# Kernel tuning notes

Hardware: AMD Instinct MI355X
Metric: run time of the kernel (lower is better)

## Reference

```python
import jax, jax.numpy as jnp
import numpy as np

DIM = 2048
HEADS = 16
HEAD_DIM = DIM // HEADS  # 128
FF = 8192
MAX_SEQ = 4096
B, S, PREV = 2, 2048, 1024
EPS = 1e-6
ROTARY_BASE = 10000.0


def setup_inputs() -> dict:
    key = jax.random.key(0)
    ks = jax.random.split(key, 16)
    n = lambda k, shape: jax.random.normal(k, shape, jnp.float32) * 0.02
    inp = {
        "x": jax.random.normal(ks[0], (B, S, DIM), jnp.float32),
        "k_cache": jax.random.normal(ks[1], (B, HEADS, PREV, HEAD_DIM), jnp.float32),
        "v_cache": jax.random.normal(ks[2], (B, HEADS, PREV, HEAD_DIM), jnp.float32),
        "attn_norm_w": jnp.ones((DIM,), jnp.float32),
        "ffn_norm_w": jnp.ones((DIM,), jnp.float32),
        "wq": n(ks[3], (DIM, DIM)), "bq": jnp.zeros((DIM,), jnp.float32),
        "wk": n(ks[4], (DIM, DIM)), "bk": jnp.zeros((DIM,), jnp.float32),
        "wv": n(ks[5], (DIM, DIM)), "bv": jnp.zeros((DIM,), jnp.float32),
        "wo": n(ks[6], (DIM, DIM)), "bo": jnp.zeros((DIM,), jnp.float32),
        "w_gate": n(ks[7], (DIM, FF)), "b_gate": jnp.zeros((FF,), jnp.float32),
        "w_val": n(ks[8], (DIM, FF)), "b_val": jnp.zeros((FF,), jnp.float32),
        "w_proj": n(ks[9], (FF, DIM)), "b_proj": jnp.zeros((DIM,), jnp.float32),
    }
    # precompute_freqs_cis as (cos, sin) pair: [MAX_SEQ, HEAD_DIM//2]
    freqs = 1.0 / (ROTARY_BASE ** (np.arange(0, HEAD_DIM, 2)[: HEAD_DIM // 2].astype(np.float32) / HEAD_DIM))
    ang = np.outer(np.arange(MAX_SEQ), freqs).astype(np.float32)
    inp["freqs_cos"] = jnp.asarray(np.cos(ang))
    inp["freqs_sin"] = jnp.asarray(np.sin(ang))
    inp["start_pos"] = PREV
    inp["cache_limit"] = 4096
    return inp


def rmsnorm(x, w):
    return x * jax.lax.rsqrt(jnp.mean(x * x, axis=-1, keepdims=True) + EPS) * w


def rope(x, cos, sin):
    # x: [B, H, S, D]; cos/sin: [1, 1, S, D/2] (complex multiply on even/odd pairs)
    xp = x.reshape(*x.shape[:-1], HEAD_DIM // 2, 2)
    x0, x1 = xp[..., 0], xp[..., 1]
    return jnp.stack([x0 * cos - x1 * sin, x0 * sin + x1 * cos], axis=-1).reshape(x.shape)


def reference(x, k_cache, v_cache, attn_norm_w, ffn_norm_w, wq, bq, wk, bk, wv, bv,
              wo, bo, w_gate, b_gate, w_val, b_val, w_proj, b_proj,
              freqs_cos, freqs_sin, start_pos, cache_limit):
    b, s, d = x.shape
    # --- attention block ---
    h = rmsnorm(x, attn_norm_w)
    split = lambda t: t.reshape(b, s, HEADS, HEAD_DIM).transpose(0, 2, 1, 3)
    q = split(h @ wq + bq)
    k = split(h @ wk + bk)
    v = split(h @ wv + bv)
    pos = (jnp.arange(s) + start_pos) % freqs_cos.shape[0]
    cos = freqs_cos[pos][None, None]  # [1,1,S,D/2]
    sin = freqs_sin[pos][None, None]
    q = rope(q, cos, sin)
    k = rope(k, cos, sin)
    # merge with KV cache (static python slicing for cache_limit)
    k_attn = jnp.concatenate([k_cache, k], axis=2)
    v_attn = jnp.concatenate([v_cache, v], axis=2)
    if cache_limit > 0:
        k_attn = k_attn[:, :, -cache_limit:, :]
        v_attn = v_attn[:, :, -cache_limit:, :]
    t_len = k_attn.shape[2]
    prev = t_len - s
    scores = jnp.einsum('bhsd,bhtd->bhst', q, k_attn) / np.float32(np.sqrt(HEAD_DIM))
    # causal mask: cache fully visible, current block lower-triangular
    allowed = jnp.arange(t_len)[None, :] <= (prev + jnp.arange(s))[:, None]
    scores = jnp.where(allowed, scores, jnp.finfo(scores.dtype).min)
    attn = jax.nn.softmax(scores, axis=-1)
    o = jnp.einsum('bhst,bhtd->bhsd', attn, v_attn).transpose(0, 2, 1, 3).reshape(b, s, d)
    x = x + (o @ wo + bo)
    # --- SwiGLU FFN block ---
    h = rmsnorm(x, ffn_norm_w)
    ff = (jax.nn.silu(h @ w_gate + b_gate) * (h @ w_val + b_val)) @ w_proj + b_proj
    x = x + ff
    return (x, k_attn, v_attn)
```

## Files before the change

### kernel.cpp

```cpp
#include <hip/hip_runtime.h>
#include <stdint.h>

typedef __bf16 bf16x8 __attribute__((ext_vector_type(8)));
typedef float  f32x4  __attribute__((ext_vector_type(4)));

__device__ __forceinline__ uint16_t f2b(float f) {
  uint32_t u = __float_as_uint(f);
  u += 0x7fffu + ((u >> 16) & 1u);
  return (uint16_t)(u >> 16);
}
__device__ __forceinline__ float b2f(uint16_t h) {
  return __uint_as_float(((uint32_t)h) << 16);
}

__device__ __forceinline__ void gl_lds16(const uint16_t* g, uint16_t* l) {
  __builtin_amdgcn_global_load_lds(
      (const __attribute__((address_space(1))) uint32_t*)g,
      (__attribute__((address_space(3))) uint32_t*)l, 16, 0, 0);
}

#define MFMA16(a,b,c) __builtin_amdgcn_mfma_f32_16x16x32_bf16((a),(b),(c),0,0,0)


__global__ __launch_bounds__(256)
void rmsnorm_k(const float* __restrict__ x, const float* __restrict__ w,
               uint16_t* __restrict__ out) {
  __shared__ float red[4];
  const int row = blockIdx.x, tid = threadIdx.x;
  const float* xr = x + (size_t)row * 2048;
  const int c = tid * 8;
  float4 a = *(const float4*)&xr[c];
  float4 b = *(const float4*)&xr[c + 4];
  float ss = a.x*a.x + a.y*a.y + a.z*a.z + a.w*a.w
           + b.x*b.x + b.y*b.y + b.z*b.z + b.w*b.w;
  ss += __shfl_xor(ss, 1);  ss += __shfl_xor(ss, 2);  ss += __shfl_xor(ss, 4);
  ss += __shfl_xor(ss, 8);  ss += __shfl_xor(ss, 16); ss += __shfl_xor(ss, 32);
  if ((tid & 63) == 0) red[tid >> 6] = ss;
  __syncthreads();
  const float tot = red[0] + red[1] + red[2] + red[3];
  const float rms = rsqrtf(tot * (1.0f / 2048.0f) + 1e-6f);
  float4 w0 = *(const float4*)&w[c];
  float4 w1 = *(const float4*)&w[c + 4];
  uint16_t* orow = out + (size_t)row * 2048;
  orow[c+0] = f2b(a.x * rms * w0.x); orow[c+1] = f2b(a.y * rms * w0.y);
  orow[c+2] = f2b(a.z * rms * w0.z); orow[c+3] = f2b(a.w * rms * w0.w);
  orow[c+4] = f2b(b.x * rms * w1.x); orow[c+5] = f2b(b.y * rms * w1.y);
  orow[c+6] = f2b(b.z * rms * w1.z); orow[c+7] = f2b(b.w * rms * w1.w);
}

__global__ void biascat_k(const float* __restrict__ bq, const float* __restrict__ bk,
                          const float* __restrict__ bv, float* __restrict__ out) {
  int i = blockIdx.x * 256 + threadIdx.x;
  if (i < 6144)
    out[i] = (i < 2048) ? bq[i] : ((i < 4096) ? bk[i - 2048] : bv[i - 4096]);
}

__global__ __launch_bounds__(256)
void transpose_k(const float* __restrict__ src, uint16_t* __restrict__ dst,
                 int K, int N) {
  __shared__ float tile[32][33];
  const int tx = threadIdx.x & 31, ty = threadIdx.x >> 5;
  const int n0 = blockIdx.x * 32, k0 = blockIdx.y * 32;
  #pragma unroll
  for (int i = 0; i < 4; ++i)
    tile[ty + i*8][tx] = src[(size_t)(k0 + ty + i*8) * N + n0 + tx];
  __syncthreads();
  #pragma unroll
  for (int i = 0; i < 4; ++i)
    dst[(size_t)(n0 + ty + i*8) * K + k0 + tx] = f2b(tile[tx][ty + i*8]);
}

__global__ __launch_bounds__(256)
void transpose_v_k(const float* __restrict__ src, uint16_t* __restrict__ dst) {
  __shared__ float tile[32][33];
  const int tx = threadIdx.x & 31, ty = threadIdx.x >> 5;
  const int t0 = blockIdx.x * 32, d0 = blockIdx.y * 32, bh = blockIdx.z;
  const float* s = src + (size_t)bh * 393216;
  uint16_t*   d = dst + (size_t)bh * 393216;
  #pragma unroll
  for (int i = 0; i < 4; ++i)
    tile[ty + i*8][tx] = s[(size_t)(t0 + ty + i*8) * 128 + d0 + tx];
  __syncthreads();
  #pragma unroll
  for (int i = 0; i < 4; ++i)
    d[(size_t)(d0 + ty + i*8) * 3072 + t0 + tx] = f2b(tile[tx][ty + i*8]);
}

__global__ __launch_bounds__(256)
void cvt_bf16_k(const float* __restrict__ src, uint16_t* __restrict__ dst) {
  const int i = blockIdx.x * 256 + threadIdx.x;
  float4 a = ((const float4*)src)[2*i];
  float4 b = ((const float4*)src)[2*i + 1];
  ushort4 lo, hi;
  lo.x = f2b(a.x); lo.y = f2b(a.y); lo.z = f2b(a.z); lo.w = f2b(a.w);
  hi.x = f2b(b.x); hi.y = f2b(b.y); hi.z = f2b(b.z); hi.w = f2b(b.w);
  ((ushort4*)dst)[2*i] = lo;
  ((ushort4*)dst)[2*i + 1] = hi;
}

__global__ __launch_bounds__(256)
void copy_cache_k(const float4* __restrict__ src, float4* __restrict__ dst) {
  const int idx = blockIdx.x * 256 + threadIdx.x;
  const int c4 = idx & 31, t = (idx >> 5) & 1023, bh = idx >> 15;
  dst[((size_t)bh * 3072 + t) * 32 + c4] = src[idx];
}

__global__ __launch_bounds__(256)
void rope_k(const uint16_t* __restrict__ qkv, const float* __restrict__ fc,
            const float* __restrict__ fs, uint16_t* __restrict__ qb,
            float* __restrict__ kat, float* __restrict__ vat) {
  const int bi = blockIdx.x;
  const int bs = bi >> 2;
  const int h  = ((bi & 3) << 2) + (threadIdx.x >> 6);
  const int d  = threadIdx.x & 63;
  const int b  = bs >> 11, s = bs & 2047;
  const int pos = s + 1024;
  const float c  = fc[pos * 64 + d];
  const float sn = fs[pos * 64 + d];
  const uint16_t* row = qkv + (size_t)bs * 6144 + h * 128;
  const float q0 = b2f(row[2*d]),        q1 = b2f(row[2*d + 1]);
  const float k0 = b2f(row[2048 + 2*d]), k1 = b2f(row[2048 + 2*d + 1]);
  const float v0 = b2f(row[4096 + 2*d]), v1 = b2f(row[4096 + 2*d + 1]);
  const size_t qo = (((size_t)b*16 + h) * 2048 + s) * 128 + 2*d;
  qb[qo]     = f2b(q0 * c - q1 * sn);
  qb[qo + 1] = f2b(q0 * sn + q1 * c);
  const size_t ko = (((size_t)b*16 + h) * 3072 + 1024 + s) * 128 + 2*d;
  kat[ko]     = k0 * c - k1 * sn;
  kat[ko + 1] = k0 * sn + k1 * c;
  vat[ko]     = v0;
  vat[ko + 1] = v1;
}

__global__ __launch_bounds__(256)
void attn_k(const uint16_t* __restrict__ qb, const uint16_t* __restrict__ kb,
            const uint16_t* __restrict__ vt, uint16_t* __restrict__ ob) {
  __shared__ __align__(16) uint16_t lsK[32 * 128];
  __shared__ __align__(16) uint16_t lsV[128 * 32];
  __shared__ __align__(16) uint16_t lsP[4][16 * 40];
  const int tid = threadIdx.x;
  const int lane = tid & 63, w = tid >> 6;
  const int l15 = lane & 15, q4 = lane >> 4;
  const int bh = blockIdx.x & 31;
  const int qi = 31 - (blockIdx.x >> 5);
  const int q0 = qi * 64;
  const int s_w = q0 + w * 16;

  int koff[2], voff[2];
  #pragma unroll
  for (int p = 0; p < 2; ++p) {
    const int idk = p * 256 + tid;
    const int krow = idk >> 4, kchp = idk & 15;
    koff[p] = krow * 128 + ((kchp ^ (krow & 15)) << 3);
    const int dd = idk >> 2, vch = idk & 3;
    voff[p] = dd * 3072 + (vch << 3);
  }
  const uint16_t* kbh = kb + (size_t)bh * 3072 * 128;
  const uint16_t* vbh = vt + (size_t)bh * 128 * 3072;

  bf16x8 qf[4];
  const uint16_t* qrow = qb + ((size_t)bh * 2048 + s_w + l15) * 128;
  #pragma unroll
  for (int kc = 0; kc < 4; ++kc)
    qf[kc] = *(const bf16x8*)&qrow[kc * 32 + q4 * 8];

  f32x4 o[8];
  #pragma unroll
  for (int nt = 0; nt < 8; ++nt) o[nt] = (f32x4){0.f, 0.f, 0.f, 0.f};
  float mrow[4], lrow[4];
  #pragma unroll
  for (int r = 0; r < 4; ++r) { mrow[r] = -1e38f; lrow[r] = 0.f; }

  const float SC = 0.08838834764831845f * 1.4426950408889634f;
  const int ntiles = (q0 + 1088) >> 5;
  const int limw = 1024 + s_w + 15;

  for (int tt = 0; tt < ntiles; ++tt) {
    const int t0 = tt << 5;
    __syncthreads();
    #pragma unroll
    for (int p = 0; p < 2; ++p) {
      gl_lds16(kbh + (size_t)t0 * 128 + koff[p], &lsK[(p * 256 + w * 64) * 8]);
      gl_lds16(vbh + t0 + voff[p],               &lsV[(p * 256 + w * 64) * 8]);
    }
    __syncthreads();
    if (t0 > limw) continue;

    f32x4 s0 = (f32x4){0.f,0.f,0.f,0.f}, s1 = (f32x4){0.f,0.f,0.f,0.f};
    #pragma unroll
    for (int kc = 0; kc < 4; ++kc) {
      const int chp = ((kc * 4 + q4) ^ l15) << 3;
      bf16x8 kf0 = *(const bf16x8*)&lsK[l15 * 128 + chp];
      bf16x8 kf1 = *(const bf16x8*)&lsK[(16 + l15) * 128 + chp];
      s0 = MFMA16(qf[kc], kf0, s0);
      s1 = MFMA16(qf[kc], kf1, s1);
    }
    if (t0 + 31 > 1024 + s_w) {
      #pragma unroll
      for (int r = 0; r < 4; ++r) {
        const int lim = 1024 + s_w + q4 * 4 + r;
        if (t0 + l15      > lim) s0[r] = -1e38f;
        if (t0 + 16 + l15 > lim) s1[r] = -1e38f;
      }
    }
    float alpha[4];
    #pragma unroll
    for (int r = 0; r < 4; ++r) {
      float v = fmaxf(s0[r], s1[r]);
      v = fmaxf(v, __shfl_xor(v, 1)); v = fmaxf(v, __shfl_xor(v, 2));
      v = fmaxf(v, __shfl_xor(v, 4)); v = fmaxf(v, __shfl_xor(v, 8));
      const float mn = fmaxf(mrow[r], v);
      alpha[r] = exp2f((mrow[r] - mn) * SC);
      mrow[r] = mn;
    }
    #pragma unroll
    for (int r = 0; r < 4; ++r) {
      const float nm = -mrow[r] * SC;
      const float p0 = exp2f(fmaf(s0[r], SC, nm));
      const float p1 = exp2f(fmaf(s1[r], SC, nm));
      float ps = p0 + p1;
      ps += __shfl_xor(ps, 1); ps += __shfl_xor(ps, 2);
      ps += __shfl_xor(ps, 4); ps += __shfl_xor(ps, 8);
      lrow[r] = fmaf(lrow[r], alpha[r], ps);
      lsP[w][(q4 * 4 + r) * 40 + l15]      = f2b(p0);
      lsP[w][(q4 * 4 + r) * 40 + 16 + l15] = f2b(p1);
    }
    #pragma unroll
    for (int nt = 0; nt < 8; ++nt)
      #pragma unroll
      for (int r = 0; r < 4; ++r) o[nt][r] *= alpha[r];
    bf16x8 pf = *(const bf16x8*)&lsP[w][l15 * 40 + q4 * 8];
    #pragma unroll
    for (int nt = 0; nt < 8; ++nt) {
      bf16x8 vf = *(const bf16x8*)&lsV[(nt * 16 + l15) * 32 + q4 * 8];
      o[nt] = MFMA16(pf, vf, o[nt]);
    }
  }
  const int b = bh >> 4, h = bh & 15;
  #pragma unroll
  for (int r = 0; r < 4; ++r) {
    const float inv = 1.0f / lrow[r];
    const int s = s_w + q4 * 4 + r;
    uint16_t* orow = ob + ((size_t)b * 2048 + s) * 2048 + h * 128;
    #pragma unroll
    for (int nt = 0; nt < 8; ++nt)
      orow[nt * 16 + l15] = f2b(o[nt][r] * inv);
  }
}

template <int EPI>
__global__ __launch_bounds__(256)
void gemm_k(const uint16_t* __restrict__ A, const uint16_t* __restrict__ Bt,
            const float* __restrict__ bias, const float* __restrict__ resid,
            const uint16_t* __restrict__ gbuf, void* __restrict__ outp,
            int M, int N, int K) {
  __shared__ __align__(16) uint16_t lsA[128 * 32];
  __shared__ __align__(16) uint16_t lsB[128 * 32];
  const int tid = threadIdx.x;
  const int lane = tid & 63, wvi = tid >> 6;
  const int l15 = lane & 15, q4 = lane >> 4;
  const int wm = wvi & 1, wn = wvi >> 1;
  const int m0 = blockIdx.y * 128, n0 = blockIdx.x * 128;
  const int lr = lane >> 2, lc = (lane & 3) << 3;

  f32x4 acc[4][4];
  #pragma unroll
  for (int i = 0; i < 4; ++i)
    #pragma unroll
    for (int j = 0; j < 4; ++j) acc[i][j] = (f32x4){0.f, 0.f, 0.f, 0.f};

  const uint16_t* Ab = A + (size_t)m0 * K;
  const uint16_t* Bb = Bt + (size_t)n0 * K;
  for (int k0 = 0; k0 < K; k0 += 32) {
    __syncthreads();
    #pragma unroll
    for (int p = 0; p < 2; ++p) {
      const int row = p * 64 + wvi * 16 + lr;
      gl_lds16(Ab + (size_t)row * K + k0 + lc, &lsA[(p * 256 + wvi * 64) * 8]);
      gl_lds16(Bb + (size_t)row * K + k0 + lc, &lsB[(p * 256 + wvi * 64) * 8]);
    }
    __syncthreads();
    bf16x8 af[4], bfr[4];
    #pragma unroll
    for (int i = 0; i < 4; ++i)
      af[i] = *(const bf16x8*)&lsA[(wm * 64 + i * 16 + l15) * 32 + q4 * 8];
    #pragma unroll
    for (int j = 0; j < 4; ++j)
      bfr[j] = *(const bf16x8*)&lsB[(wn * 64 + j * 16 + l15) * 32 + q4 * 8];
    #pragma unroll
    for (int i = 0; i < 4; ++i)
      #pragma unroll
      for (int j = 0; j < 4; ++j)
        acc[i][j] = MFMA16(af[i], bfr[j], acc[i][j]);
  }
  #pragma unroll
  for (int i = 0; i < 4; ++i) {
    #pragma unroll
    for (int j = 0; j < 4; ++j) {
      const int n = n0 + wn * 64 + j * 16 + l15;
      const float bn = bias[n];
      #pragma unroll
      for (int r = 0; r < 4; ++r) {
        const int m = m0 + wm * 64 + i * 16 + q4 * 4 + r;
        const size_t off = (size_t)m * N + n;
        const float v = acc[i][j][r] + bn;
        if (EPI == 0) {
          ((uint16_t*)outp)[off] = f2b(v);
        } else if (EPI == 1) {
          ((float*)outp)[off] = v + resid[off];
        } else {
          const float g = b2f(gbuf[off]);
          const float sg = g / (1.0f + __expf(-g));
          ((uint16_t*)outp)[off] = f2b(sg * v);
        }
      }
    }
  }
}

extern "C" void kernel_launch(void* const* d_in, const int* in_sizes, int n_in,
                              void* d_out, int out_size, void* d_ws, size_t ws_size,
                              hipStream_t stream) {
  const float* x   = (const float*)d_in[0];
  const float* kc  = (const float*)d_in[1];
  const float* vc  = (const float*)d_in[2];
  const float* anw = (const float*)d_in[3];
  const float* fnw = (const float*)d_in[4];
  const float* wq  = (const float*)d_in[5];
  const float* bq  = (const float*)d_in[6];
  const float* wk  = (const float*)d_in[7];
  const float* bk  = (const float*)d_in[8];
  const float* wv_ = (const float*)d_in[9];
  const float* bv  = (const float*)d_in[10];
  const float* wo  = (const float*)d_in[11];
  const float* bo  = (const float*)d_in[12];
  const float* wg  = (const float*)d_in[13];
  const float* bg  = (const float*)d_in[14];
  const float* wva = (const float*)d_in[15];
  const float* bva = (const float*)d_in[16];
  const float* wp  = (const float*)d_in[17];
  const float* bp  = (const float*)d_in[18];
  const float* fc  = (const float*)d_in[19];
  const float* fs  = (const float*)d_in[20];

  float* out_x = (float*)d_out;
  float* kat = out_x + 8388608;
  float* vat = kat + 12582912;

  char* ws = (char*)d_ws;
  uint16_t* h_b   = (uint16_t*)(ws);
  uint16_t* wbuf  = (uint16_t*)(ws + 16777216);
  uint16_t* qkv_b = (uint16_t*)(ws + 50331648);
  uint16_t* k_b   = (uint16_t*)(ws + 50331648);
  uint16_t* v_t   = (uint16_t*)(ws + 75497472);
  uint16_t* q_b   = (uint16_t*)(ws + 100663296);
  uint16_t* o_b   = (uint16_t*)(ws + 117440512);
  float*    x1    = (float*)   (ws + 134217728);
  float*    bcat  = (float*)   (ws + 167772160);
  uint16_t* g_b   = qkv_b;

  rmsnorm_k<<<4096, 256, 0, stream>>>(x, anw, h_b);
  biascat_k<<<24, 256, 0, stream>>>(bq, bk, bv, bcat);
  transpose_k<<<dim3(64, 64), 256, 0, stream>>>(wq,  wbuf,               2048, 2048);
  transpose_k<<<dim3(64, 64), 256, 0, stream>>>(wk,  wbuf + 1*2048*2048, 2048, 2048);
  transpose_k<<<dim3(64, 64), 256, 0, stream>>>(wv_, wbuf + 2*2048*2048, 2048, 2048);
  gemm_k<0><<<dim3(48, 32), 256, 0, stream>>>(h_b, wbuf, bcat, nullptr, nullptr,
                                              (void*)qkv_b, 4096, 6144, 2048);
  copy_cache_k<<<4096, 256, 0, stream>>>((const float4*)kc, (float4*)kat);
  copy_cache_k<<<4096, 256, 0, stream>>>((const float4*)vc, (float4*)vat);
  rope_k<<<16384, 256, 0, stream>>>(qkv_b, fc, fs, q_b, kat, vat);
  cvt_bf16_k<<<6144, 256, 0, stream>>>(kat, k_b);
  transpose_v_k<<<dim3(96, 4, 32), 256, 0, stream>>>(vat, v_t);
  attn_k<<<1024, 256, 0, stream>>>(q_b, k_b, v_t, o_b);
  transpose_k<<<dim3(64, 64), 256, 0, stream>>>(wo, wbuf, 2048, 2048);
  gemm_k<1><<<dim3(16, 32), 256, 0, stream>>>(o_b, wbuf, bo, x, nullptr,
                                              (void*)x1, 4096, 2048, 2048);
  rmsnorm_k<<<4096, 256, 0, stream>>>(x1, fnw, h_b);
  transpose_k<<<dim3(256, 64), 256, 0, stream>>>(wg, wbuf, 2048, 8192);
  gemm_k<0><<<dim3(64, 32), 256, 0, stream>>>(h_b, wbuf, bg, nullptr, nullptr,
                                              (void*)g_b, 4096, 8192, 2048);
  transpose_k<<<dim3(256, 64), 256, 0, stream>>>(wva, wbuf, 2048, 8192);
  gemm_k<2><<<dim3(64, 32), 256, 0, stream>>>(h_b, wbuf, bva, nullptr, g_b,
                                              (void*)g_b, 4096, 8192, 2048);
  transpose_k<<<dim3(64, 256), 256, 0, stream>>>(wp, wbuf, 8192, 2048);
  gemm_k<1><<<dim3(16, 32), 256, 0, stream>>>(g_b, wbuf, bp, x1, nullptr,
                                              (void*)out_x, 4096, 2048, 8192);
}
```

Measured before the change: 1.471 ms.

## Widen attention KV tile to 64, fuse K bf16 conversion into copy and rope

The attention kernel now processes 64 keys per tile instead of 32. It uses four score MFMAs and two PV MFMAs per d-tile, XOR-swizzles the V layout in LDS, defers the row-sum reduction to the end, and skips the output rescale when no lane's max changed. The separate fp32-to-bf16 pass over the whole K cache is removed: the bf16 K copy is now written directly by the cache-copy kernel and by rope_k, and the workspace buffers are relocated to fit. This cuts one full read and write of K and halves the number of attention barriers, at the cost of more LDS, more registers and more masked work on the diagonal tile.

```diff
diff --git a/kernel.cpp b/kernel.cpp
--- a/kernel.cpp
+++ b/kernel.cpp
@@ -87,18 +87,6 @@
 }
 
 __global__ __launch_bounds__(256)
-void cvt_bf16_k(const float* __restrict__ src, uint16_t* __restrict__ dst) {
-  const int i = blockIdx.x * 256 + threadIdx.x;
-  float4 a = ((const float4*)src)[2*i];
-  float4 b = ((const float4*)src)[2*i + 1];
-  ushort4 lo, hi;
-  lo.x = f2b(a.x); lo.y = f2b(a.y); lo.z = f2b(a.z); lo.w = f2b(a.w);
-  hi.x = f2b(b.x); hi.y = f2b(b.y); hi.z = f2b(b.z); hi.w = f2b(b.w);
-  ((ushort4*)dst)[2*i] = lo;
-  ((ushort4*)dst)[2*i + 1] = hi;
-}
-
-__global__ __launch_bounds__(256)
 void copy_cache_k(const float4* __restrict__ src, float4* __restrict__ dst) {
   const int idx = blockIdx.x * 256 + threadIdx.x;
   const int c4 = idx & 31, t = (idx >> 5) & 1023, bh = idx >> 15;
@@ -106,9 +94,23 @@
 }
 
 __global__ __launch_bounds__(256)
+void copy_cache_kb_k(const float4* __restrict__ src, float4* __restrict__ dst,
+                     uint16_t* __restrict__ dstb) {
+  const int idx = blockIdx.x * 256 + threadIdx.x;
+  const int c4 = idx & 31, t = (idx >> 5) & 1023, bh = idx >> 15;
+  float4 v = src[idx];
+  const size_t o = ((size_t)bh * 3072 + t) * 32 + c4;
+  dst[o] = v;
+  ushort4 b;
+  b.x = f2b(v.x); b.y = f2b(v.y); b.z = f2b(v.z); b.w = f2b(v.w);
+  ((ushort4*)dstb)[o] = b;
+}
+
+__global__ __launch_bounds__(256)
 void rope_k(const uint16_t* __restrict__ qkv, const float* __restrict__ fc,
             const float* __restrict__ fs, uint16_t* __restrict__ qb,
-            float* __restrict__ kat, float* __restrict__ vat) {
+            float* __restrict__ kat, float* __restrict__ vat,
+            uint16_t* __restrict__ kbb) {
   const int bi = blockIdx.x;
   const int bs = bi >> 2;
   const int h  = ((bi & 3) << 2) + (threadIdx.x >> 6);
@@ -125,8 +127,12 @@
   qb[qo]     = f2b(q0 * c - q1 * sn);
   qb[qo + 1] = f2b(q0 * sn + q1 * c);
   const size_t ko = (((size_t)b*16 + h) * 3072 + 1024 + s) * 128 + 2*d;
-  kat[ko]     = k0 * c - k1 * sn;
-  kat[ko + 1] = k0 * sn + k1 * c;
+  const float kr0 = k0 * c - k1 * sn;
+  const float kr1 = k0 * sn + k1 * c;
+  kat[ko]     = kr0;
+  kat[ko + 1] = kr1;
+  kbb[ko]     = f2b(kr0);
+  kbb[ko + 1] = f2b(kr1);
   vat[ko]     = v0;
   vat[ko + 1] = v1;
 }
@@ -134,9 +140,9 @@
 __global__ __launch_bounds__(256)
 void attn_k(const uint16_t* __restrict__ qb, const uint16_t* __restrict__ kb,
             const uint16_t* __restrict__ vt, uint16_t* __restrict__ ob) {
-  __shared__ __align__(16) uint16_t lsK[32 * 128];
-  __shared__ __align__(16) uint16_t lsV[128 * 32];
-  __shared__ __align__(16) uint16_t lsP[4][16 * 40];
+  __shared__ __align__(16) uint16_t lsK[64 * 128];
+  __shared__ __align__(16) uint16_t lsV[128 * 64];
+  __shared__ __align__(16) uint16_t lsP[4][16 * 72];
   const int tid = threadIdx.x;
   const int lane = tid & 63, w = tid >> 6;
   const int l15 = lane & 15, q4 = lane >> 4;
@@ -145,14 +151,14 @@
   const int q0 = qi * 64;
   const int s_w = q0 + w * 16;
 
-  int koff[2], voff[2];
-  #pragma unroll
-  for (int p = 0; p < 2; ++p) {
+  int koff[4], voff[4];
+  #pragma unroll
+  for (int p = 0; p < 4; ++p) {
     const int idk = p * 256 + tid;
-    const int krow = idk >> 4, kchp = idk & 15;
-    koff[p] = krow * 128 + ((kchp ^ (krow & 15)) << 3);
-    const int dd = idk >> 2, vch = idk & 3;
-    voff[p] = dd * 3072 + (vch << 3);
+    const int krow = idk >> 4, kch = idk & 15;
+    koff[p] = krow * 128 + ((kch ^ (krow & 15)) << 3);
+    const int dd = idk >> 3, vch = idk & 7;
+    voff[p] = dd * 3072 + ((vch ^ (dd & 7)) << 3);
   }
   const uint16_t* kbh = kb + (size_t)bh * 3072 * 128;
   const uint16_t* vbh = vt + (size_t)bh * 128 * 3072;
@@ -171,41 +177,49 @@
   for (int r = 0; r < 4; ++r) { mrow[r] = -1e38f; lrow[r] = 0.f; }
 
   const float SC = 0.08838834764831845f * 1.4426950408889634f;
-  const int ntiles = (q0 + 1088) >> 5;
+  const int ntiles = qi + 17;
   const int limw = 1024 + s_w + 15;
 
   for (int tt = 0; tt < ntiles; ++tt) {
-    const int t0 = tt << 5;
+    const int t0 = tt << 6;
     __syncthreads();
     #pragma unroll
-    for (int p = 0; p < 2; ++p) {
+    for (int p = 0; p < 4; ++p) {
       gl_lds16(kbh + (size_t)t0 * 128 + koff[p], &lsK[(p * 256 + w * 64) * 8]);
       gl_lds16(vbh + t0 + voff[p],               &lsV[(p * 256 + w * 64) * 8]);
     }
     __syncthreads();
     if (t0 > limw) continue;
 
-    f32x4 s0 = (f32x4){0.f,0.f,0.f,0.f}, s1 = (f32x4){0.f,0.f,0.f,0.f};
+    f32x4 s[4];
+    #pragma unroll
+    for (int kg = 0; kg < 4; ++kg) s[kg] = (f32x4){0.f,0.f,0.f,0.f};
     #pragma unroll
     for (int kc = 0; kc < 4; ++kc) {
       const int chp = ((kc * 4 + q4) ^ l15) << 3;
-      bf16x8 kf0 = *(const bf16x8*)&lsK[l15 * 128 + chp];
+      bf16x8 kf0 = *(const bf16x8*)&lsK[ l15       * 128 + chp];
       bf16x8 kf1 = *(const bf16x8*)&lsK[(16 + l15) * 128 + chp];
-      s0 = MFMA16(qf[kc], kf0, s0);
-      s1 = MFMA16(qf[kc], kf1, s1);
-    }
-    if (t0 + 31 > 1024 + s_w) {
+      bf16x8 kf2 = *(const bf16x8*)&lsK[(32 + l15) * 128 + chp];
+      bf16x8 kf3 = *(const bf16x8*)&lsK[(48 + l15) * 128 + chp];
+      s[0] = MFMA16(qf[kc], kf0, s[0]);
+      s[1] = MFMA16(qf[kc], kf1, s[1]);
+      s[2] = MFMA16(qf[kc], kf2, s[2]);
+      s[3] = MFMA16(qf[kc], kf3, s[3]);
+    }
+    if (t0 + 63 > 1024 + s_w) {
       #pragma unroll
       for (int r = 0; r < 4; ++r) {
         const int lim = 1024 + s_w + q4 * 4 + r;
-        if (t0 + l15      > lim) s0[r] = -1e38f;
-        if (t0 + 16 + l15 > lim) s1[r] = -1e38f;
+        if (t0 +      l15 > lim) s[0][r] = -1e38f;
+        if (t0 + 16 + l15 > lim) s[1][r] = -1e38f;
+        if (t0 + 32 + l15 > lim) s[2][r] = -1e38f;
+        if (t0 + 48 + l15 > lim) s[3][r] = -1e38f;
       }
     }
     float alpha[4];
     #pragma unroll
     for (int r = 0; r < 4; ++r) {
-      float v = fmaxf(s0[r], s1[r]);
+      float v = fmaxf(fmaxf(s[0][r], s[1][r]), fmaxf(s[2][r], s[3][r]));
       v = fmaxf(v, __shfl_xor(v, 1)); v = fmaxf(v, __shfl_xor(v, 2));
       v = fmaxf(v, __shfl_xor(v, 4)); v = fmaxf(v, __shfl_xor(v, 8));
       const float mn = fmaxf(mrow[r], v);
@@ -215,30 +229,42 @@
     #pragma unroll
     for (int r = 0; r < 4; ++r) {
       const float nm = -mrow[r] * SC;
-      const float p0 = exp2f(fmaf(s0[r], SC, nm));
-      const float p1 = exp2f(fmaf(s1[r], SC, nm));
-      float ps = p0 + p1;
-      ps += __shfl_xor(ps, 1); ps += __shfl_xor(ps, 2);
-      ps += __shfl_xor(ps, 4); ps += __shfl_xor(ps, 8);
-      lrow[r] = fmaf(lrow[r], alpha[r], ps);
-      lsP[w][(q4 * 4 + r) * 40 + l15]      = f2b(p0);
-      lsP[w][(q4 * 4 + r) * 40 + 16 + l15] = f2b(p1);
-    }
-    #pragma unroll
-    for (int nt = 0; nt < 8; ++nt)
+      const float p0 = exp2f(fmaf(s[0][r], SC, nm));
+      const float p1 = exp2f(fmaf(s[1][r], SC, nm));
+      const float p2 = exp2f(fmaf(s[2][r], SC, nm));
+      const float p3 = exp2f(fmaf(s[3][r], SC, nm));
+      lrow[r] = fmaf(lrow[r], alpha[r], (p0 + p1) + (p2 + p3));
+      const int pr = (q4 * 4 + r) * 72;
+      lsP[w][pr +      l15] = f2b(p0);
+      lsP[w][pr + 16 + l15] = f2b(p1);
+      lsP[w][pr + 32 + l15] = f2b(p2);
+      lsP[w][pr + 48 + l15] = f2b(p3);
+    }
+    const float as = alpha[0] * alpha[1] * alpha[2] * alpha[3];
+    if (__any(as != 1.0f)) {
       #pragma unroll
-      for (int r = 0; r < 4; ++r) o[nt][r] *= alpha[r];
-    bf16x8 pf = *(const bf16x8*)&lsP[w][l15 * 40 + q4 * 8];
+      for (int nt = 0; nt < 8; ++nt)
+        #pragma unroll
+        for (int r = 0; r < 4; ++r) o[nt][r] *= alpha[r];
+    }
+    bf16x8 pf0 = *(const bf16x8*)&lsP[w][l15 * 72      + q4 * 8];
+    bf16x8 pf1 = *(const bf16x8*)&lsP[w][l15 * 72 + 32 + q4 * 8];
     #pragma unroll
     for (int nt = 0; nt < 8; ++nt) {
-      bf16x8 vf = *(const bf16x8*)&lsV[(nt * 16 + l15) * 32 + q4 * 8];
-      o[nt] = MFMA16(pf, vf, o[nt]);
+      const int d = nt * 16 + l15;
+      bf16x8 vf0 = *(const bf16x8*)&lsV[d * 64 + (( q4      ^ (d & 7)) << 3)];
+      bf16x8 vf1 = *(const bf16x8*)&lsV[d * 64 + (((4 + q4) ^ (d & 7)) << 3)];
+      o[nt] = MFMA16(pf0, vf0, o[nt]);
+      o[nt] = MFMA16(pf1, vf1, o[nt]);
     }
   }
   const int b = bh >> 4, h = bh & 15;
   #pragma unroll
   for (int r = 0; r < 4; ++r) {
-    const float inv = 1.0f / lrow[r];
+    float l = lrow[r];
+    l += __shfl_xor(l, 1); l += __shfl_xor(l, 2);
+    l += __shfl_xor(l, 4); l += __shfl_xor(l, 8);
+    const float inv = 1.0f / l;
     const int s = s_w + q4 * 4 + r;
     uint16_t* orow = ob + ((size_t)b * 2048 + s) * 2048 + h * 128;
     #pragma unroll
@@ -349,9 +375,9 @@
   char* ws = (char*)d_ws;
   uint16_t* h_b   = (uint16_t*)(ws);
   uint16_t* wbuf  = (uint16_t*)(ws + 16777216);
+  uint16_t* k_b   = (uint16_t*)(ws);
+  uint16_t* v_t   = (uint16_t*)(ws + 25165824);
   uint16_t* qkv_b = (uint16_t*)(ws + 50331648);
-  uint16_t* k_b   = (uint16_t*)(ws + 50331648);
-  uint16_t* v_t   = (uint16_t*)(ws + 75497472);
   uint16_t* q_b   = (uint16_t*)(ws + 100663296);
   uint16_t* o_b   = (uint16_t*)(ws + 117440512);
   float*    x1    = (float*)   (ws + 134217728);
@@ -365,10 +391,9 @@
   transpose_k<<<dim3(64, 64), 256, 0, stream>>>(wv_, wbuf + 2*2048*2048, 2048, 2048);
   gemm_k<0><<<dim3(48, 32), 256, 0, stream>>>(h_b, wbuf, bcat, nullptr, nullptr,
                                               (void*)qkv_b, 4096, 6144, 2048);
-  copy_cache_k<<<4096, 256, 0, stream>>>((const float4*)kc, (float4*)kat);
+  copy_cache_kb_k<<<4096, 256, 0, stream>>>((const float4*)kc, (float4*)kat, k_b);
   copy_cache_k<<<4096, 256, 0, stream>>>((const float4*)vc, (float4*)vat);
-  rope_k<<<16384, 256, 0, stream>>>(qkv_b, fc, fs, q_b, kat, vat);
-  cvt_bf16_k<<<6144, 256, 0, stream>>>(kat, k_b);
+  rope_k<<<16384, 256, 0, stream>>>(qkv_b, fc, fs, q_b, kat, vat, k_b);
   transpose_v_k<<<dim3(96, 4, 32), 256, 0, stream>>>(vat, v_t);
   attn_k<<<1024, 256, 0, stream>>>(q_b, k_b, v_t, o_b);
   transpose_k<<<dim3(64, 64), 256, 0, stream>>>(wo, wbuf, 2048, 2048);
```

Measured after the change: 1.384 ms. 1.06x faster.
